# Kernel optimization log

Measured on AMD Instinct MI355X. Metric: run time of the kernel, lower is better.

## Reference

```python
import jax, jax.numpy as jnp
import numpy as np

CONF_T = 0.9      # confidence_threshold
NMS_T = 0.4       # nms_threshold
VAR0, VAR1 = 0.1, 0.2  # variances
SCALE = 2048.0    # image size used in decode_bbox
K = 512           # fixed candidate cap for jit-friendly NMS
N = 2_097_152     # number of priors


def setup_inputs() -> dict:
    key = jax.random.key(0)
    k1, k2, k3 = jax.random.split(key, 3)
    loc = jax.random.normal(k1, (1, N, 4), dtype=jnp.float32)
    conf = jax.random.normal(k2, (1, N, 2), dtype=jnp.float32)
    priors = jax.random.uniform(k3, (N, 4), dtype=jnp.float32)  # normalized cx,cy,w,h
    return {"loc": loc, "conf": conf, "priors": priors}


def _decode(loc, priors):
    # standard SSD decode: loc [N,4], priors [N,4] (cx,cy,w,h) -> boxes [N,4] (x1,y1,x2,y2)
    cxcy = priors[:, :2] + loc[:, :2] * VAR0 * priors[:, 2:]
    wh = priors[:, 2:] * jnp.exp(loc[:, 2:] * VAR1)
    x1y1 = cxcy - wh * 0.5
    x2y2 = x1y1 + wh
    return jnp.concatenate([x1y1, x2y2], axis=-1)


def _pairwise_iou(b):
    # b: [K,4] in pixel coords; py_cpu_nms convention with +1 on widths/heights
    area = (b[:, 2] - b[:, 0] + 1.0) * (b[:, 3] - b[:, 1] + 1.0)  # [K]
    xx1 = jnp.maximum(b[:, None, 0], b[None, :, 0])
    yy1 = jnp.maximum(b[:, None, 1], b[None, :, 1])
    xx2 = jnp.minimum(b[:, None, 2], b[None, :, 2])
    yy2 = jnp.minimum(b[:, None, 3], b[None, :, 3])
    w = jnp.maximum(xx2 - xx1 + 1.0, 0.0)
    h = jnp.maximum(yy2 - yy1 + 1.0, 0.0)
    inter = w * h
    return inter / (area[:, None] + area[None, :] - inter)


def reference(loc, conf, priors):
    boxes = _decode(loc[0], priors) * SCALE                     # [N,4] pixel coords
    scores = jax.nn.softmax(conf[0], axis=-1)[:, 1]             # [N] face scores
    # threshold: invalid -> -1 so top_k pushes them to the end
    s = jnp.where(scores > CONF_T, scores, -1.0)
    top_s, idx = jax.lax.top_k(s, K)                            # sorted desc = argsort order
    cand = boxes[idx]                                           # [K,4]
    iou = _pairwise_iou(cand)                                   # [K,K]
    keep0 = top_s > 0.0                                         # only thresholded candidates
    ar = jnp.arange(K)
    def body(i, keep):
        sup = keep[i] & (iou[i] > NMS_T) & (ar > i)             # suppress lower-scored overlaps
        return keep & ~sup
    keep = jax.lax.fori_loop(0, K, body, keep0)
    dets = jnp.concatenate([cand / SCALE, top_s[:, None]], axis=-1)  # [K,5], boxes renormalized
    return jnp.where(keep[:, None], dets, 0.0)                  # zero-padded fixed-shape dets
```

## Files before the change

### kernel.cpp

```cpp
#include <hip/hip_runtime.h>
#include <stdint.h>

#define N_PRIORS 2097152
#define KTOP 512
#define NBINS 2048
#define K1BLK 2048
#define SCAP 32
#define SELCAP 2048
#define SSTASH 0.9915f
#define NSUPB 16


__device__ __forceinline__ uint64_t pack_key(float s, int idx) {
    return ((uint64_t)__float_as_uint(s) << 32) | (uint32_t)(~idx);
}

__device__ __forceinline__ float score_of(float c0, float c1) {
    #pragma clang fp contract(off)
    float m  = fmaxf(c0, c1);
    float e0 = expf(c0 - m);
    float e1 = expf(c1 - m);
    return e1 / (e0 + e1);
}

__device__ __forceinline__ int bin_of(float s) {
    #pragma clang fp contract(off)
    int b = (int)((s - 0.9f) * 20480.0f);
    return b > (NBINS - 1) ? (NBINS - 1) : b;
}

__device__ __forceinline__ uint64_t shfl_xor64(uint64_t x, int mask) {
    int lo = __shfl_xor((int)(uint32_t)x, mask, 64);
    int hi = __shfl_xor((int)(uint32_t)(x >> 32), mask, 64);
    return ((uint64_t)(uint32_t)hi << 32) | (uint32_t)lo;
}

__device__ __forceinline__ float4 decode_box(int idx,
                                             const float4* __restrict__ loc,
                                             const float4* __restrict__ priors) {
    #pragma clang fp contract(off)
    float4 l = loc[idx];
    float4 p = priors[idx];
    float cx = p.x + (l.x * 0.1f) * p.z;
    float cy = p.y + (l.y * 0.1f) * p.w;
    float w  = p.z * expf(l.z * 0.2f);
    float h  = p.w * expf(l.w * 0.2f);
    float x1 = cx - w * 0.5f;
    float y1 = cy - h * 0.5f;
    float x2 = x1 + w;
    float y2 = y1 + h;
    x1 *= 2048.0f; y1 *= 2048.0f; x2 *= 2048.0f; y2 *= 2048.0f;
    return make_float4(x1, y1, x2, y2);
}

__global__ void k1_stash(const float4* __restrict__ conf4,
                         const float4* __restrict__ loc,
                         const float4* __restrict__ priors,
                         uint32_t* __restrict__ blk_cnt,
                         uint64_t* __restrict__ key_stash,
                         float4* __restrict__ box_stash,
                         uint32_t* __restrict__ done_g) {
    #pragma clang fp contract(off)
    __shared__ uint32_t lcnt;
    int t = threadIdx.x;
    int blk = blockIdx.x;
    if (blk == 0 && t == 0) *done_g = 0u;
    if (t == 0) lcnt = 0;
    __syncthreads();
    uint64_t* kreg = key_stash + (size_t)blk * SCAP;
    float4*   breg = box_stash + (size_t)blk * SCAP;
    #pragma unroll
    for (int i = 0; i < 2; ++i) {
        int f4i = blk * 512 + t + 256 * i;
        float4 c = conf4[f4i];
        float s0 = score_of(c.x, c.y);
        float s1 = score_of(c.z, c.w);
        if (s0 > SSTASH) {
            uint32_t p = atomicAdd(&lcnt, 1u);
            if (p < SCAP) {
                kreg[p] = pack_key(s0, f4i * 2);
                breg[p] = decode_box(f4i * 2, loc, priors);
            }
        }
        if (s1 > SSTASH) {
            uint32_t p = atomicAdd(&lcnt, 1u);
            if (p < SCAP) {
                kreg[p] = pack_key(s1, f4i * 2 + 1);
                breg[p] = decode_box(f4i * 2 + 1, loc, priors);
            }
        }
    }
    __syncthreads();
    if (t == 0) blk_cnt[blk] = (lcnt <= SCAP) ? lcnt : 0xFFFFFFFFu;
}

__launch_bounds__(1024)
__global__ void k2_fused(const float4* __restrict__ loc,
                         const float4* __restrict__ priors,
                         const float4* __restrict__ conf4,
                         const uint32_t* __restrict__ blk_cnt,
                         const uint64_t* __restrict__ key_stash,
                         const float4* __restrict__ box_stash,
                         uint32_t* done_g,
                         uint32_t* rowany_g,
                         uint64_t* supW_g,
                         float* __restrict__ out) {
    #pragma clang fp contract(off)
    __shared__ uint64_t arena[4096];
    uint64_t* sel  = arena;
    uint32_t* slt  = (uint32_t*)(arena + 2048);
    uint64_t* supW = arena;
    __shared__ float4 bbxL[SELCAP];
    __shared__ uint32_t hist[NBINS];
    __shared__ float4 bpk[KTOP];
    __shared__ float  sar[KTOP], ssc[KTOP];
    __shared__ uint64_t keepw0[8];
    __shared__ uint64_t keepw[8];
    __shared__ uint32_t rowanyL[16];
    __shared__ uint32_t nselS, fbS, anyS, tailS;
    __shared__ int bmaxS;

    int tid = threadIdx.x;
    int lane = tid & 63, wv = tid >> 6;

    if (tid == 0) { nselS = 0u; fbS = 0u; anyS = 0u; bmaxS = 0; }
    __syncthreads();

    for (int b = tid; b < K1BLK; b += 1024) {
        uint32_t c = blk_cnt[b];
        if (c == 0xFFFFFFFFu) { atomicOr(&fbS, 1u); c = 0; }
        uint32_t base = 0;
        if (c > 0) base = atomicAdd(&nselS, c);
        for (uint32_t j = 0; j < c; ++j) {
            uint32_t p = base + j;
            if (p < SELCAP) {
                sel[p]  = key_stash[(size_t)b * SCAP + j];
                bbxL[p] = box_stash[(size_t)b * SCAP + j];
                slt[p]  = p;
            } else {
                atomicOr(&fbS, 1u);
            }
        }
    }
    __syncthreads();
    uint32_t n = nselS;
    bool fb = (fbS != 0u) || (n < KTOP) || (n > SELCAP);
    __syncthreads();

    if (fb) {
        if (tid == 0) nselS = 0u;
        for (int b = tid; b < NBINS; b += 1024) hist[b] = 0u;
        __syncthreads();
        for (int f = tid; f < N_PRIORS / 2; f += 1024) {
            float4 c = conf4[f];
            float s0 = score_of(c.x, c.y);
            float s1 = score_of(c.z, c.w);
            if (s0 > 0.9f) atomicAdd(&hist[bin_of(s0)], 1u);
            if (s1 > 0.9f) atomicAdd(&hist[bin_of(s1)], 1u);
        }
        __syncthreads();
        for (int off = 1; off < NBINS; off <<= 1) {
            int b0 = tid, b1 = tid + 1024;
            uint32_t v0 = hist[b0] + ((b0 + off < NBINS) ? hist[b0 + off] : 0u);
            uint32_t v1 = hist[b1] + ((b1 + off < NBINS) ? hist[b1 + off] : 0u);
            __syncthreads();
            hist[b0] = v0; hist[b1] = v1;
            __syncthreads();
        }
        if (hist[tid] >= KTOP) atomicMax(&bmaxS, tid);
        if (hist[tid + 1024] >= KTOP) atomicMax(&bmaxS, tid + 1024);
        __syncthreads();
        int B = bmaxS;
        for (int f = tid; f < N_PRIORS / 2; f += 1024) {
            float4 c = conf4[f];
            float s0 = score_of(c.x, c.y);
            float s1 = score_of(c.z, c.w);
            if (s0 > 0.9f && bin_of(s0) >= B) {
                uint32_t p = atomicAdd(&nselS, 1u);
                if (p < SELCAP) { sel[p] = pack_key(s0, 2 * f); slt[p] = p; }
            }
            if (s1 > 0.9f && bin_of(s1) >= B) {
                uint32_t p = atomicAdd(&nselS, 1u);
                if (p < SELCAP) { sel[p] = pack_key(s1, 2 * f + 1); slt[p] = p; }
            }
        }
        __syncthreads();
        n = nselS; if (n > SELCAP) n = SELCAP;
        __syncthreads();
    }

    int P = KTOP; while (P < (int)n) P <<= 1;
    for (int t = tid; t < P; t += 1024)
        if (t >= (int)n) { sel[t] = 0ull; slt[t] = 0u; }
    __syncthreads();

    uint64_t v;
    uint32_t sl;

    if (P <= 1024) {
        v  = (tid < P) ? sel[tid] : 0ull;
        sl = (tid < P) ? slt[tid] : 0u;
        for (int k = 2; k <= P; k <<= 1) {
            for (int j = k >> 1; j >= 64; j >>= 1) {
                if (tid < P) { sel[tid] = v; slt[tid] = sl; }
                __syncthreads();
                if (tid < P) {
                    uint64_t pv = sel[tid ^ j];
                    uint32_t ps = slt[tid ^ j];
                    bool wmax = (((tid & j) == 0) == ((tid & k) == 0));
                    bool take = wmax ? (pv > v) : (pv < v);
                    if (take) { v = pv; sl = ps; }
                }
                __syncthreads();
            }
            int j0 = (k >> 1) < 32 ? (k >> 1) : 32;
            for (int j = j0; j >= 1; j >>= 1) {
                uint64_t pv = shfl_xor64(v, j);
                uint32_t ps = (uint32_t)__shfl_xor((int)sl, j, 64);
                bool wmax = (((tid & j) == 0) == ((tid & k) == 0));
                bool take = wmax ? (pv > v) : (pv < v);
                v = take ? pv : v; sl = take ? ps : sl;
            }
        }
    } else {
        for (int k = 2; k <= P; k <<= 1) {
            for (int j = k >> 1; j > 0; j >>= 1) {
                for (int t = tid; t < P; t += 1024) {
                    int ixj = t ^ j;
                    if (ixj > t) {
                        uint64_t a = sel[t], b = sel[ixj];
                        bool sw = ((t & k) == 0) ? (a < b) : (a > b);
                        if (sw) {
                            sel[t] = b; sel[ixj] = a;
                            uint32_t sa = slt[t]; slt[t] = slt[ixj]; slt[ixj] = sa;
                        }
                    }
                }
                __syncthreads();
            }
        }
        v  = (tid < KTOP) ? sel[tid] : 0ull;
        sl = (tid < KTOP) ? slt[tid] : 0u;
    }

    {
        uint64_t key = (tid < KTOP) ? v : 0ull;
        if (tid < KTOP) {
            float4 bb; float area, sc;
            if (key != 0ull) {
                sc = __uint_as_float((uint32_t)(key >> 32));
                if (!fb) {
                    bb = bbxL[sl];
                } else {
                    int idx = (int)(~(uint32_t)key);
                    bb = decode_box(idx, loc, priors);
                }
                area = (bb.z - bb.x + 1.0f) * (bb.w - bb.y + 1.0f);
            } else {
                bb = make_float4(0.f, 0.f, 0.f, 0.f); area = 1.f; sc = 0.f;
            }
            bpk[tid] = bb; sar[tid] = area; ssc[tid] = sc;
        }
        uint64_t vb = __ballot(key != 0ull);
        if (lane == 0 && wv < 8) keepw0[wv] = vb;
    }
    __syncthreads();

    {
        float4 cb0 = bpk[lane +   0], cb1 = bpk[lane +  64];
        float4 cb2 = bpk[lane + 128], cb3 = bpk[lane + 192];
        float4 cb4 = bpk[lane + 256], cb5 = bpk[lane + 320];
        float4 cb6 = bpk[lane + 384], cb7 = bpk[lane + 448];
        float ca0 = (cb0.z - cb0.x + 1.0f) * (cb0.w - cb0.y + 1.0f);
        float ca1 = (cb1.z - cb1.x + 1.0f) * (cb1.w - cb1.y + 1.0f);
        float ca2 = (cb2.z - cb2.x + 1.0f) * (cb2.w - cb2.y + 1.0f);
        float ca3 = (cb3.z - cb3.x + 1.0f) * (cb3.w - cb3.y + 1.0f);
        float ca4 = (cb4.z - cb4.x + 1.0f) * (cb4.w - cb4.y + 1.0f);
        float ca5 = (cb5.z - cb5.x + 1.0f) * (cb5.w - cb5.y + 1.0f);
        float ca6 = (cb6.z - cb6.x + 1.0f) * (cb6.w - cb6.y + 1.0f);
        float ca7 = (cb7.z - cb7.x + 1.0f) * (cb7.w - cb7.y + 1.0f);
        #define SUPC(c, CB, CA) do { \
            float xx1 = fmaxf(rb.x, CB.x); float yy1 = fmaxf(rb.y, CB.y); \
            float xx2 = fminf(rb.z, CB.z); float yy2 = fminf(rb.w, CB.w); \
            float ww = fmaxf(xx2 - xx1 + 1.0f, 0.0f); \
            float hh = fmaxf(yy2 - yy1 + 1.0f, 0.0f); \
            float inter = ww * hh; \
            float iou = inter / (ra + (CA) - inter); \
            uint64_t wrd = __ballot(iou > 0.4f && (64 * (c) + lane) > r); \
            if (lane == 0) supW_g[r * 8 + (c)] = wrd; \
            any |= wrd; } while (0)
        uint32_t mybits = 0u;
        int rbase = blockIdx.x * 32 + wv * 2;
        for (int rr = 0; rr < 2; ++rr) {
            int r = rbase + rr;
            float4 rb = bpk[r];
            float ra = sar[r];
            uint64_t any = 0ull;
            SUPC(0, cb0, ca0); SUPC(1, cb1, ca1); SUPC(2, cb2, ca2); SUPC(3, cb3, ca3);
            SUPC(4, cb4, ca4); SUPC(5, cb5, ca5); SUPC(6, cb6, ca6); SUPC(7, cb7, ca7);
            if (lane == 0 && any != 0ull) mybits |= 1u << (r & 31);
        }
        #undef SUPC
        if (lane == 0 && mybits != 0u) atomicOr(&anyS, mybits);
    }
    __syncthreads();

    if (tid == 0) {
        rowany_g[blockIdx.x] = anyS;
        __threadfence();
        uint32_t old = atomicAdd(done_g, 1u);
        tailS = (old == (uint32_t)(NSUPB - 1)) ? 1u : 0u;
    }
    __syncthreads();
    if (tailS == 0u) return;

    __threadfence();
    for (int i = tid; i < KTOP * 8; i += 1024)
        supW[i] = __hip_atomic_load(&supW_g[i], __ATOMIC_RELAXED,
                                    __HIP_MEMORY_SCOPE_AGENT);
    if (tid < 16)
        rowanyL[tid] = __hip_atomic_load(&rowany_g[tid], __ATOMIC_RELAXED,
                                         __HIP_MEMORY_SCOPE_AGENT);
    __syncthreads();

    if (tid == 0) {
        #define RA64(c) (((uint64_t)rowanyL[2*(c)]) | (((uint64_t)rowanyL[2*(c)+1]) << 32))
        uint64_t kp0 = keepw0[0], kp1 = keepw0[1], kp2 = keepw0[2], kp3 = keepw0[3];
        uint64_t kp4 = keepw0[4], kp5 = keepw0[5], kp6 = keepw0[6], kp7 = keepw0[7];
        #define APPLYROW(i) do { const uint64_t* rp = supW + (size_t)(i) * 8; \
            kp0 &= ~rp[0]; kp1 &= ~rp[1]; kp2 &= ~rp[2]; kp3 &= ~rp[3]; \
            kp4 &= ~rp[4]; kp5 &= ~rp[5]; kp6 &= ~rp[6]; kp7 &= ~rp[7]; } while (0)
        #define CHUNK(c, KPC) do { uint64_t ra = RA64(c); uint64_t m = (KPC) & ra; \
            while (m) { int b = __builtin_ctzll(m); APPLYROW((c) * 64 + b); \
                uint64_t above = (b == 63) ? 0ull : (~0ull << (b + 1)); \
                m = (KPC) & ra & above; } } while (0)
        CHUNK(0, kp0); CHUNK(1, kp1); CHUNK(2, kp2); CHUNK(3, kp3);
        CHUNK(4, kp4); CHUNK(5, kp5); CHUNK(6, kp6); CHUNK(7, kp7);
        keepw[0] = kp0; keepw[1] = kp1; keepw[2] = kp2; keepw[3] = kp3;
        keepw[4] = kp4; keepw[5] = kp5; keepw[6] = kp6; keepw[7] = kp7;
        #undef CHUNK
        #undef APPLYROW
        #undef RA64
    }
    __syncthreads();

    if (tid < KTOP) {
        const float inv = 1.0f / 2048.0f;
        int kb = (int)((keepw[tid >> 6] >> (tid & 63)) & 1ull);
        float4 bb = bpk[tid];
        float* o = out + tid * 5;
        if (kb) {
            o[0] = bb.x * inv;
            o[1] = bb.y * inv;
            o[2] = bb.z * inv;
            o[3] = bb.w * inv;
            o[4] = ssc[tid];
        } else {
            o[0] = 0.f; o[1] = 0.f; o[2] = 0.f; o[3] = 0.f; o[4] = 0.f;
        }
    }
}

extern "C" void kernel_launch(void* const* d_in, const int* in_sizes, int n_in,
                              void* d_out, int out_size, void* d_ws, size_t ws_size,
                              hipStream_t stream) {
    const float* loc    = (const float*)d_in[0];
    const float* conf   = (const float*)d_in[1];
    const float* priors = (const float*)d_in[2];
    float* out = (float*)d_out;

    uint8_t* ws = (uint8_t*)d_ws;
    uint32_t* blk_cnt   = (uint32_t*)ws;
    uint64_t* key_stash = (uint64_t*)(ws + 8192);
    float4*   box_stash = (float4*)(ws + 532480);
    uint32_t* done_g    = (uint32_t*)(ws + 1581056);
    uint32_t* rowany_g  = (uint32_t*)(ws + 1581120);
    uint64_t* supW_g    = (uint64_t*)(ws + 1581184);

    k1_stash<<<K1BLK, 256, 0, stream>>>((const float4*)conf,
                                        (const float4*)loc,
                                        (const float4*)priors,
                                        blk_cnt, key_stash, box_stash, done_g);
    k2_fused<<<NSUPB, 1024, 0, stream>>>((const float4*)loc, (const float4*)priors,
                                         (const float4*)conf, blk_cnt,
                                         key_stash, box_stash,
                                         done_g, rowany_g, supW_g, out);
}
```

Baseline: 140.0 us.

## Replace per-block stash with 64 global-atomic segments and compact gather

The first kernel now appends candidates directly into 64 segment buffers (32 blocks each) using global atomics, instead of per-block LDS counters feeding 2048 fixed slots. The fused kernel therefore only scans 64 counters with a serial prefix and gathers at most 4096 slots, rather than walking 2048 block counts with atomics. Boxes are read from global memory at selection time instead of being staged in shared memory. The workspace is cleared with an extra memset launch, and contended global atomics in the first kernel may add cost there.

```diff
diff --git a/kernel.cpp b/kernel.cpp
--- a/kernel.cpp
+++ b/kernel.cpp
@@ -5,7 +5,8 @@
 #define KTOP 512
 #define NBINS 2048
 #define K1BLK 2048
-#define SCAP 32
+#define NSEG 64
+#define SEGCAP 64
 #define SELCAP 2048
 #define SSTASH 0.9915f
 #define NSUPB 16
@@ -53,22 +54,16 @@
     return make_float4(x1, y1, x2, y2);
 }
 
-__global__ void k1_stash(const float4* __restrict__ conf4,
-                         const float4* __restrict__ loc,
-                         const float4* __restrict__ priors,
-                         uint32_t* __restrict__ blk_cnt,
-                         uint64_t* __restrict__ key_stash,
-                         float4* __restrict__ box_stash,
-                         uint32_t* __restrict__ done_g) {
-    #pragma clang fp contract(off)
-    __shared__ uint32_t lcnt;
+__global__ void k1_emit(const float4* __restrict__ conf4,
+                        const float4* __restrict__ loc,
+                        const float4* __restrict__ priors,
+                        uint32_t* __restrict__ seg_cnt,
+                        uint64_t* __restrict__ keys_seg,
+                        float4* __restrict__ box_seg) {
+    #pragma clang fp contract(off)
     int t = threadIdx.x;
     int blk = blockIdx.x;
-    if (blk == 0 && t == 0) *done_g = 0u;
-    if (t == 0) lcnt = 0;
-    __syncthreads();
-    uint64_t* kreg = key_stash + (size_t)blk * SCAP;
-    float4*   breg = box_stash + (size_t)blk * SCAP;
+    int g = blk >> 5;
     #pragma unroll
     for (int i = 0; i < 2; ++i) {
         int f4i = blk * 512 + t + 256 * i;
@@ -76,31 +71,29 @@
         float s0 = score_of(c.x, c.y);
         float s1 = score_of(c.z, c.w);
         if (s0 > SSTASH) {
-            uint32_t p = atomicAdd(&lcnt, 1u);
-            if (p < SCAP) {
-                kreg[p] = pack_key(s0, f4i * 2);
-                breg[p] = decode_box(f4i * 2, loc, priors);
+            uint32_t p = atomicAdd(&seg_cnt[g], 1u);
+            if (p < SEGCAP) {
+                keys_seg[g * SEGCAP + p] = pack_key(s0, f4i * 2);
+                box_seg[g * SEGCAP + p]  = decode_box(f4i * 2, loc, priors);
             }
         }
         if (s1 > SSTASH) {
-            uint32_t p = atomicAdd(&lcnt, 1u);
-            if (p < SCAP) {
-                kreg[p] = pack_key(s1, f4i * 2 + 1);
-                breg[p] = decode_box(f4i * 2 + 1, loc, priors);
-            }
-        }
-    }
-    __syncthreads();
-    if (t == 0) blk_cnt[blk] = (lcnt <= SCAP) ? lcnt : 0xFFFFFFFFu;
+            uint32_t p = atomicAdd(&seg_cnt[g], 1u);
+            if (p < SEGCAP) {
+                keys_seg[g * SEGCAP + p] = pack_key(s1, f4i * 2 + 1);
+                box_seg[g * SEGCAP + p]  = decode_box(f4i * 2 + 1, loc, priors);
+            }
+        }
+    }
 }
 
 __launch_bounds__(1024)
 __global__ void k2_fused(const float4* __restrict__ loc,
                          const float4* __restrict__ priors,
                          const float4* __restrict__ conf4,
-                         const uint32_t* __restrict__ blk_cnt,
-                         const uint64_t* __restrict__ key_stash,
-                         const float4* __restrict__ box_stash,
+                         const uint32_t* __restrict__ seg_cnt,
+                         const uint64_t* __restrict__ keys_seg,
+                         const float4* __restrict__ box_seg,
                          uint32_t* done_g,
                          uint32_t* rowany_g,
                          uint64_t* supW_g,
@@ -110,13 +103,14 @@
     uint64_t* sel  = arena;
     uint32_t* slt  = (uint32_t*)(arena + 2048);
     uint64_t* supW = arena;
-    __shared__ float4 bbxL[SELCAP];
     __shared__ uint32_t hist[NBINS];
     __shared__ float4 bpk[KTOP];
     __shared__ float  sar[KTOP], ssc[KTOP];
     __shared__ uint64_t keepw0[8];
     __shared__ uint64_t keepw[8];
     __shared__ uint32_t rowanyL[16];
+    __shared__ uint32_t scnt[NSEG];
+    __shared__ uint32_t segoff[NSEG];
     __shared__ uint32_t nselS, fbS, anyS, tailS;
     __shared__ int bmaxS;
 
@@ -124,30 +118,34 @@
     int lane = tid & 63, wv = tid >> 6;
 
     if (tid == 0) { nselS = 0u; fbS = 0u; anyS = 0u; bmaxS = 0; }
-    __syncthreads();
-
-    for (int b = tid; b < K1BLK; b += 1024) {
-        uint32_t c = blk_cnt[b];
-        if (c == 0xFFFFFFFFu) { atomicOr(&fbS, 1u); c = 0; }
-        uint32_t base = 0;
-        if (c > 0) base = atomicAdd(&nselS, c);
-        for (uint32_t j = 0; j < c; ++j) {
-            uint32_t p = base + j;
-            if (p < SELCAP) {
-                sel[p]  = key_stash[(size_t)b * SCAP + j];
-                bbxL[p] = box_stash[(size_t)b * SCAP + j];
-                slt[p]  = p;
-            } else {
-                atomicOr(&fbS, 1u);
-            }
-        }
+    if (tid < NSEG) scnt[tid] = seg_cnt[tid];
+    __syncthreads();
+
+    if (tid == 0) {
+        uint32_t acc = 0u, ov = 0u;
+        for (int g = 0; g < NSEG; ++g) {
+            segoff[g] = acc;
+            uint32_t c = scnt[g];
+            if (c > SEGCAP) { ov = 1u; c = SEGCAP; }
+            acc += c;
+        }
+        nselS = acc; fbS = ov;
     }
     __syncthreads();
     uint32_t n = nselS;
     bool fb = (fbS != 0u) || (n < KTOP) || (n > SELCAP);
     __syncthreads();
 
-    if (fb) {
+    if (!fb) {
+        for (int t = tid; t < NSEG * SEGCAP; t += 1024) {
+            int g = t >> 6, s = t & (SEGCAP - 1);
+            if ((uint32_t)s < scnt[g]) {
+                uint32_t p = segoff[g] + (uint32_t)s;
+                sel[p] = keys_seg[t];
+                slt[p] = (uint32_t)t;
+            }
+        }
+    } else {
         if (tid == 0) nselS = 0u;
         for (int b = tid; b < NBINS; b += 1024) hist[b] = 0u;
         __syncthreads();
@@ -188,6 +186,7 @@
         n = nselS; if (n > SELCAP) n = SELCAP;
         __syncthreads();
     }
+    __syncthreads();
 
     int P = KTOP; while (P < (int)n) P <<= 1;
     for (int t = tid; t < P; t += 1024)
@@ -250,7 +249,7 @@
             if (key != 0ull) {
                 sc = __uint_as_float((uint32_t)(key >> 32));
                 if (!fb) {
-                    bb = bbxL[sl];
+                    bb = box_seg[sl];
                 } else {
                     int idx = (int)(~(uint32_t)key);
                     bb = decode_box(idx, loc, priors);
@@ -370,19 +369,20 @@
     float* out = (float*)d_out;
 
     uint8_t* ws = (uint8_t*)d_ws;
-    uint32_t* blk_cnt   = (uint32_t*)ws;
-    uint64_t* key_stash = (uint64_t*)(ws + 8192);
-    float4*   box_stash = (float4*)(ws + 532480);
-    uint32_t* done_g    = (uint32_t*)(ws + 1581056);
-    uint32_t* rowany_g  = (uint32_t*)(ws + 1581120);
-    uint64_t* supW_g    = (uint64_t*)(ws + 1581184);
-
-    k1_stash<<<K1BLK, 256, 0, stream>>>((const float4*)conf,
-                                        (const float4*)loc,
-                                        (const float4*)priors,
-                                        blk_cnt, key_stash, box_stash, done_g);
+    uint32_t* seg_cnt  = (uint32_t*)ws;
+    uint32_t* done_g   = (uint32_t*)(ws + 256);
+    uint64_t* keys_seg = (uint64_t*)(ws + 512);
+    float4*   box_seg  = (float4*)(ws + 33280);
+    uint32_t* rowany_g = (uint32_t*)(ws + 98816);
+    uint64_t* supW_g   = (uint64_t*)(ws + 98944);
+
+    hipMemsetAsync(ws, 0, 512, stream);
+    k1_emit<<<K1BLK, 256, 0, stream>>>((const float4*)conf,
+                                       (const float4*)loc,
+                                       (const float4*)priors,
+                                       seg_cnt, keys_seg, box_seg);
     k2_fused<<<NSUPB, 1024, 0, stream>>>((const float4*)loc, (const float4*)priors,
-                                         (const float4*)conf, blk_cnt,
-                                         key_stash, box_stash,
+                                         (const float4*)conf, seg_cnt,
+                                         keys_seg, box_seg,
                                          done_g, rowany_g, supW_g, out);
 }
```

Result: no change. 141.0 us (+0.7%).

## Collapse NMS to single block with prefix-scan gather and larger stash blocks

Applied to the files above, without the earlier changes.

The stash kernel now uses 512 blocks of 1024 threads with a 16-entry cap per block instead of 2048 blocks of 256 threads. The NMS kernel runs as one block instead of 16 cooperating blocks. A prefix scan over the block counts replaces the atomic gather, so candidate order is deterministic. The suppression matrix stays in shared memory and each wave computes 32 rows, which removes the global last-block handoff, threadfences and global atomics. In exchange, the single block does all 512 IoU rows serially per wave, and the smaller per-block cap makes the slow full-scan fallback more likely.

```diff
diff --git a/kernel.cpp b/kernel.cpp
--- a/kernel.cpp
+++ b/kernel.cpp
@@ -4,11 +4,10 @@
 #define N_PRIORS 2097152
 #define KTOP 512
 #define NBINS 2048
-#define K1BLK 2048
-#define SCAP 32
+#define K1BLK 512
+#define BCAP 16
 #define SELCAP 2048
 #define SSTASH 0.9915f
-#define NSUPB 16
 
 
 __device__ __forceinline__ uint64_t pack_key(float s, int idx) {
@@ -53,101 +52,109 @@
     return make_float4(x1, y1, x2, y2);
 }
 
-__global__ void k1_stash(const float4* __restrict__ conf4,
-                         const float4* __restrict__ loc,
-                         const float4* __restrict__ priors,
-                         uint32_t* __restrict__ blk_cnt,
-                         uint64_t* __restrict__ key_stash,
-                         float4* __restrict__ box_stash,
-                         uint32_t* __restrict__ done_g) {
+__launch_bounds__(1024)
+__global__ void k1_emit(const float4* __restrict__ conf4,
+                        const float4* __restrict__ loc,
+                        const float4* __restrict__ priors,
+                        uint32_t* __restrict__ cnt_g,
+                        uint64_t* __restrict__ keys_g,
+                        float4* __restrict__ box_g) {
     #pragma clang fp contract(off)
     __shared__ uint32_t lcnt;
     int t = threadIdx.x;
     int blk = blockIdx.x;
-    if (blk == 0 && t == 0) *done_g = 0u;
     if (t == 0) lcnt = 0;
     __syncthreads();
-    uint64_t* kreg = key_stash + (size_t)blk * SCAP;
-    float4*   breg = box_stash + (size_t)blk * SCAP;
+    uint64_t* kreg = keys_g + (size_t)blk * BCAP;
+    float4*   breg = box_g  + (size_t)blk * BCAP;
     #pragma unroll
     for (int i = 0; i < 2; ++i) {
-        int f4i = blk * 512 + t + 256 * i;
+        int f4i = blk * 2048 + t + 1024 * i;
         float4 c = conf4[f4i];
         float s0 = score_of(c.x, c.y);
         float s1 = score_of(c.z, c.w);
         if (s0 > SSTASH) {
             uint32_t p = atomicAdd(&lcnt, 1u);
-            if (p < SCAP) {
+            if (p < BCAP) {
                 kreg[p] = pack_key(s0, f4i * 2);
                 breg[p] = decode_box(f4i * 2, loc, priors);
             }
         }
         if (s1 > SSTASH) {
             uint32_t p = atomicAdd(&lcnt, 1u);
-            if (p < SCAP) {
+            if (p < BCAP) {
                 kreg[p] = pack_key(s1, f4i * 2 + 1);
                 breg[p] = decode_box(f4i * 2 + 1, loc, priors);
             }
         }
     }
     __syncthreads();
-    if (t == 0) blk_cnt[blk] = (lcnt <= SCAP) ? lcnt : 0xFFFFFFFFu;
+    if (t == 0) cnt_g[blk] = (lcnt <= BCAP) ? lcnt : 0xFFFFFFFFu;
 }
 
 __launch_bounds__(1024)
-__global__ void k2_fused(const float4* __restrict__ loc,
-                         const float4* __restrict__ priors,
-                         const float4* __restrict__ conf4,
-                         const uint32_t* __restrict__ blk_cnt,
-                         const uint64_t* __restrict__ key_stash,
-                         const float4* __restrict__ box_stash,
-                         uint32_t* done_g,
-                         uint32_t* rowany_g,
-                         uint64_t* supW_g,
-                         float* __restrict__ out) {
-    #pragma clang fp contract(off)
-    __shared__ uint64_t arena[4096];
-    uint64_t* sel  = arena;
-    uint32_t* slt  = (uint32_t*)(arena + 2048);
-    uint64_t* supW = arena;
-    __shared__ float4 bbxL[SELCAP];
-    __shared__ uint32_t hist[NBINS];
+__global__ void k2_nms(const float4* __restrict__ loc,
+                       const float4* __restrict__ priors,
+                       const float4* __restrict__ conf4,
+                       const uint32_t* __restrict__ cnt_g,
+                       const uint64_t* __restrict__ keys_g,
+                       const float4* __restrict__ box_g,
+                       float* __restrict__ out) {
+    #pragma clang fp contract(off)
+    __shared__ uint64_t sortbuf[4096];
+    uint64_t* sel  = sortbuf;
+    uint32_t* slt  = (uint32_t*)(sortbuf + 2048);
+    uint64_t* supW = sortbuf;
+    __shared__ float4 bxArena[2048];
+    float4*   bxL  = bxArena;
+    uint32_t* hist = (uint32_t*)bxArena;
     __shared__ float4 bpk[KTOP];
     __shared__ float  sar[KTOP], ssc[KTOP];
+    __shared__ uint32_t scnt[K1BLK];
+    __shared__ uint32_t pfx[K1BLK];
     __shared__ uint64_t keepw0[8];
     __shared__ uint64_t keepw[8];
-    __shared__ uint32_t rowanyL[16];
-    __shared__ uint32_t nselS, fbS, anyS, tailS;
+    __shared__ uint32_t rowany32[16];
+    __shared__ uint32_t nselS, fbS;
     __shared__ int bmaxS;
 
     int tid = threadIdx.x;
     int lane = tid & 63, wv = tid >> 6;
 
-    if (tid == 0) { nselS = 0u; fbS = 0u; anyS = 0u; bmaxS = 0; }
-    __syncthreads();
-
-    for (int b = tid; b < K1BLK; b += 1024) {
-        uint32_t c = blk_cnt[b];
-        if (c == 0xFFFFFFFFu) { atomicOr(&fbS, 1u); c = 0; }
-        uint32_t base = 0;
-        if (c > 0) base = atomicAdd(&nselS, c);
-        for (uint32_t j = 0; j < c; ++j) {
-            uint32_t p = base + j;
-            if (p < SELCAP) {
-                sel[p]  = key_stash[(size_t)b * SCAP + j];
-                bbxL[p] = box_stash[(size_t)b * SCAP + j];
-                slt[p]  = p;
-            } else {
-                atomicOr(&fbS, 1u);
-            }
-        }
-    }
+    if (tid == 0) { nselS = 0u; fbS = 0u; bmaxS = 0; }
+    if (tid < 16) rowany32[tid] = 0u;
+    if (tid < K1BLK) scnt[tid] = cnt_g[tid];
+    __syncthreads();
+    if (tid < K1BLK) {
+        uint32_t c = scnt[tid];
+        if (c > BCAP) { atomicOr(&fbS, 1u); c = 0u; }
+        scnt[tid] = c; pfx[tid] = c;
+    }
+    __syncthreads();
+    for (int off = 1; off < K1BLK; off <<= 1) {
+        uint32_t add = 0u;
+        if (tid < K1BLK && tid >= off) add = pfx[tid - off];
+        __syncthreads();
+        if (tid < K1BLK) pfx[tid] += add;
+        __syncthreads();
+    }
+    if (tid == 0) nselS = pfx[K1BLK - 1];
     __syncthreads();
     uint32_t n = nselS;
     bool fb = (fbS != 0u) || (n < KTOP) || (n > SELCAP);
     __syncthreads();
 
-    if (fb) {
+    if (!fb) {
+        for (int t0 = tid; t0 < K1BLK * BCAP; t0 += 1024) {
+            int g = t0 >> 4, s = t0 & (BCAP - 1);
+            uint32_t c = scnt[g];
+            if ((uint32_t)s < c) {
+                uint32_t p = pfx[g] - c + (uint32_t)s;
+                sel[p] = keys_g[t0];
+                bxL[p] = box_g[t0];
+            }
+        }
+    } else {
         if (tid == 0) nselS = 0u;
         for (int b = tid; b < NBINS; b += 1024) hist[b] = 0u;
         __syncthreads();
@@ -177,21 +184,24 @@
             float s1 = score_of(c.z, c.w);
             if (s0 > 0.9f && bin_of(s0) >= B) {
                 uint32_t p = atomicAdd(&nselS, 1u);
-                if (p < SELCAP) { sel[p] = pack_key(s0, 2 * f); slt[p] = p; }
+                if (p < SELCAP) sel[p] = pack_key(s0, 2 * f);
             }
             if (s1 > 0.9f && bin_of(s1) >= B) {
                 uint32_t p = atomicAdd(&nselS, 1u);
-                if (p < SELCAP) { sel[p] = pack_key(s1, 2 * f + 1); slt[p] = p; }
+                if (p < SELCAP) sel[p] = pack_key(s1, 2 * f + 1);
             }
         }
         __syncthreads();
         n = nselS; if (n > SELCAP) n = SELCAP;
         __syncthreads();
     }
+    __syncthreads();
 
     int P = KTOP; while (P < (int)n) P <<= 1;
-    for (int t = tid; t < P; t += 1024)
-        if (t >= (int)n) { sel[t] = 0ull; slt[t] = 0u; }
+    for (int t0 = tid; t0 < P; t0 += 1024) {
+        if (t0 >= (int)n) sel[t0] = 0ull;
+        slt[t0] = (uint32_t)t0;
+    }
     __syncthreads();
 
     uint64_t v;
@@ -225,14 +235,14 @@
     } else {
         for (int k = 2; k <= P; k <<= 1) {
             for (int j = k >> 1; j > 0; j >>= 1) {
-                for (int t = tid; t < P; t += 1024) {
-                    int ixj = t ^ j;
-                    if (ixj > t) {
-                        uint64_t a = sel[t], b = sel[ixj];
-                        bool sw = ((t & k) == 0) ? (a < b) : (a > b);
+                for (int t0 = tid; t0 < P; t0 += 1024) {
+                    int ixj = t0 ^ j;
+                    if (ixj > t0) {
+                        uint64_t a = sel[t0], b = sel[ixj];
+                        bool sw = ((t0 & k) == 0) ? (a < b) : (a > b);
                         if (sw) {
-                            sel[t] = b; sel[ixj] = a;
-                            uint32_t sa = slt[t]; slt[t] = slt[ixj]; slt[ixj] = sa;
+                            sel[t0] = b; sel[ixj] = a;
+                            uint32_t sa = slt[t0]; slt[t0] = slt[ixj]; slt[ixj] = sa;
                         }
                     }
                 }
@@ -250,7 +260,7 @@
             if (key != 0ull) {
                 sc = __uint_as_float((uint32_t)(key >> 32));
                 if (!fb) {
-                    bb = bbxL[sl];
+                    bb = bxL[sl];
                 } else {
                     int idx = (int)(~(uint32_t)key);
                     bb = decode_box(idx, loc, priors);
@@ -287,44 +297,26 @@
             float inter = ww * hh; \
             float iou = inter / (ra + (CA) - inter); \
             uint64_t wrd = __ballot(iou > 0.4f && (64 * (c) + lane) > r); \
-            if (lane == 0) supW_g[r * 8 + (c)] = wrd; \
+            if (lane == 0) supW[r * 8 + (c)] = wrd; \
             any |= wrd; } while (0)
         uint32_t mybits = 0u;
-        int rbase = blockIdx.x * 32 + wv * 2;
-        for (int rr = 0; rr < 2; ++rr) {
+        int rbase = wv * 32;
+        for (int rr = 0; rr < 32; ++rr) {
             int r = rbase + rr;
             float4 rb = bpk[r];
             float ra = sar[r];
             uint64_t any = 0ull;
             SUPC(0, cb0, ca0); SUPC(1, cb1, ca1); SUPC(2, cb2, ca2); SUPC(3, cb3, ca3);
             SUPC(4, cb4, ca4); SUPC(5, cb5, ca5); SUPC(6, cb6, ca6); SUPC(7, cb7, ca7);
-            if (lane == 0 && any != 0ull) mybits |= 1u << (r & 31);
+            if (lane == 0 && any != 0ull) mybits |= 1u << rr;
         }
         #undef SUPC
-        if (lane == 0 && mybits != 0u) atomicOr(&anyS, mybits);
+        if (lane == 0) rowany32[wv] = mybits;
     }
     __syncthreads();
 
     if (tid == 0) {
-        rowany_g[blockIdx.x] = anyS;
-        __threadfence();
-        uint32_t old = atomicAdd(done_g, 1u);
-        tailS = (old == (uint32_t)(NSUPB - 1)) ? 1u : 0u;
-    }
-    __syncthreads();
-    if (tailS == 0u) return;
-
-    __threadfence();
-    for (int i = tid; i < KTOP * 8; i += 1024)
-        supW[i] = __hip_atomic_load(&supW_g[i], __ATOMIC_RELAXED,
-                                    __HIP_MEMORY_SCOPE_AGENT);
-    if (tid < 16)
-        rowanyL[tid] = __hip_atomic_load(&rowany_g[tid], __ATOMIC_RELAXED,
-                                         __HIP_MEMORY_SCOPE_AGENT);
-    __syncthreads();
-
-    if (tid == 0) {
-        #define RA64(c) (((uint64_t)rowanyL[2*(c)]) | (((uint64_t)rowanyL[2*(c)+1]) << 32))
+        #define RA64(c) (((uint64_t)rowany32[2*(c)]) | (((uint64_t)rowany32[2*(c)+1]) << 32))
         uint64_t kp0 = keepw0[0], kp1 = keepw0[1], kp2 = keepw0[2], kp3 = keepw0[3];
         uint64_t kp4 = keepw0[4], kp5 = keepw0[5], kp6 = keepw0[6], kp7 = keepw0[7];
         #define APPLYROW(i) do { const uint64_t* rp = supW + (size_t)(i) * 8; \
@@ -370,19 +362,14 @@
     float* out = (float*)d_out;
 
     uint8_t* ws = (uint8_t*)d_ws;
-    uint32_t* blk_cnt   = (uint32_t*)ws;
-    uint64_t* key_stash = (uint64_t*)(ws + 8192);
-    float4*   box_stash = (float4*)(ws + 532480);
-    uint32_t* done_g    = (uint32_t*)(ws + 1581056);
-    uint32_t* rowany_g  = (uint32_t*)(ws + 1581120);
-    uint64_t* supW_g    = (uint64_t*)(ws + 1581184);
-
-    k1_stash<<<K1BLK, 256, 0, stream>>>((const float4*)conf,
+    uint32_t* cnt_g  = (uint32_t*)ws;
+    uint64_t* keys_g = (uint64_t*)(ws + 2048);
+    float4*   box_g  = (float4*)(ws + 67584);
+
+    k1_emit<<<K1BLK, 1024, 0, stream>>>((const float4*)conf,
                                         (const float4*)loc,
                                         (const float4*)priors,
-                                        blk_cnt, key_stash, box_stash, done_g);
-    k2_fused<<<NSUPB, 1024, 0, stream>>>((const float4*)loc, (const float4*)priors,
-                                         (const float4*)conf, blk_cnt,
-                                         key_stash, box_stash,
-                                         done_g, rowany_g, supW_g, out);
-}
+                                        cnt_g, keys_g, box_g);
+    k2_nms<<<1, 1024, 0, stream>>>((const float4*)loc, (const float4*)priors,
+                                   (const float4*)conf, cnt_g, keys_g, box_g, out);
+}
```

Measured after the change: 176.7 us. 1.26x slower.
